# Kernel tuning notes

Measured on AMD Instinct MI355X. Metric: run time of the kernel, lower is better.

Reference implementation:

```python
import jax, jax.numpy as jnp
import numpy as np
import math

DIM_IN, DIM_CTX, DIM_KEY, DIM_VAL = 2048, 512, 128, 128
N, T, H, W = 8, 16, 32, 32
NBOX = 512


def setup_inputs() -> dict:
    key = jax.random.key(0)
    ks = jax.random.split(key, 10)
    rois = jax.random.normal(ks[0], (NBOX, DIM_IN), dtype=jnp.float32)
    context = jax.random.normal(ks[1], (N, DIM_CTX, T, H, W), dtype=jnp.float32)
    batch_idx = jnp.sort(jax.random.randint(ks[2], (NBOX,), 0, N))
    s = 0.02
    W_proj = jax.random.normal(ks[3], (DIM_KEY, DIM_IN), dtype=jnp.float32) * s
    b_proj = jnp.zeros((DIM_KEY,), dtype=jnp.float32)
    W_keys = jax.random.normal(ks[4], (DIM_KEY, DIM_CTX), dtype=jnp.float32) * s
    b_keys = jnp.zeros((DIM_KEY,), dtype=jnp.float32)
    W_vals = jax.random.normal(ks[5], (DIM_VAL, DIM_CTX), dtype=jnp.float32) * s
    b_vals = jnp.zeros((DIM_VAL,), dtype=jnp.float32)
    return {"rois": rois, "context": context, "batch_idx": batch_idx,
            "W_proj": W_proj, "b_proj": b_proj,
            "W_keys": W_keys, "b_keys": b_keys,
            "W_vals": W_vals, "b_vals": b_vals}


def reference(rois, context, batch_idx, W_proj, b_proj, W_keys, b_keys, W_vals, b_vals):
    n, c, t, h, w = context.shape
    s = t * h * w
    dk = W_keys.shape[0]
    # ROI query projection: [Nb, dk]
    q = rois @ W_proj.T + b_proj
    # 1x1x1 Conv3d == per-voxel linear over channels
    ctx_flat = context.reshape(n, c, s)                       # [N, C, S]
    keys = jnp.einsum('kc,ncs->nks', W_keys, ctx_flat) + b_keys[None, :, None]  # [N, dk, S]
    vals = jnp.einsum('vc,ncs->nsv', W_vals, ctx_flat) + b_vals[None, None, :]  # [N, S, dv]
    # Per-box gather of its clip's keys/vals, fused cross-attention
    qk = jnp.einsum('bk,bks->bs', q, keys[batch_idx]) / math.sqrt(dk)  # [Nb, S]
    coeff = jax.nn.softmax(qk, axis=-1)
    ctx_out = jnp.einsum('bs,bsv->bv', coeff, vals[batch_idx])         # [Nb, dv]
    attn = coeff.reshape(-1, t, h, w) * 255.0
    return ctx_out, attn
```

## Files before the change

### kernel.cpp

```cpp
#include <hip/hip_runtime.h>
#include <hip/hip_bf16.h>
#include <math.h>

#define DIM_IN  2048
#define DIM_CTX 512
#define DIM_KEY 128
#define DIM_VAL 128
#define NCLIP   8
#define S_TOT   16384
#define NBOX    512
#define MAXB    96

typedef __attribute__((ext_vector_type(8))) short short8_t;
typedef __attribute__((ext_vector_type(4))) float f32x4;

__device__ inline unsigned short f2bf(float x) {
    union { float f; unsigned int u; } v; v.f = x;
    unsigned int r = v.u + 0x7FFFu + ((v.u >> 16) & 1u);
    return (unsigned short)(r >> 16);
}
__device__ inline float bf2f(unsigned short h) {
    union { unsigned int u; float f; } v; v.u = ((unsigned int)h) << 16;
    return v.f;
}

__global__ __launch_bounds__(256) void k0_init(const int* __restrict__ batch_idx,
                                               int* __restrict__ ranges,
                                               float* __restrict__ cctx) {
    int idx = blockIdx.x * blockDim.x + threadIdx.x;
    for (int i = idx; i < NBOX * DIM_CTX; i += gridDim.x * blockDim.x)
        cctx[i] = 0.0f;
    if (blockIdx.x == 0) {
        __shared__ int s_start[NCLIP], s_end[NCLIP];
        if (threadIdx.x < NCLIP) { s_start[threadIdx.x] = NBOX; s_end[threadIdx.x] = 0; }
        __syncthreads();
        for (int i = threadIdx.x; i < NBOX; i += blockDim.x) {
            int b = batch_idx[i];
            atomicMin(&s_start[b], i);
            atomicMax(&s_end[b], i + 1);
        }
        __syncthreads();
        if (threadIdx.x < NCLIP) {
            ranges[threadIdx.x]         = s_start[threadIdx.x];
            ranges[NCLIP + threadIdx.x] = s_end[threadIdx.x];
        }
    }
}

__global__ __launch_bounds__(256) void conv_ctx(const float* __restrict__ ctx,
                                                unsigned short* __restrict__ ctxB,
                                                unsigned short* __restrict__ ctxT) {
    int n = blockIdx.z;
    int c0 = blockIdx.y * 64;
    int sch = blockIdx.x * 128;
    int t = threadIdx.x;
    __shared__ float ls[64 * 132];
    const float* src = ctx + ((size_t)n * DIM_CTX + c0) * S_TOT + sch;
    unsigned short* dstB = ctxB + ((size_t)n * DIM_CTX + c0) * S_TOT + sch;
    #pragma unroll
    for (int r = 0; r < 8; ++r) {
        int idx = t + r * 256;
        int c_l = idx >> 5, s4 = (idx & 31) * 4;
        float4 v = *(const float4*)(src + (size_t)c_l * S_TOT + s4);
        *(float4*)&ls[c_l * 132 + s4] = v;
        uint2 pk;
        pk.x = f2bf(v.x) | ((unsigned)f2bf(v.y) << 16);
        pk.y = f2bf(v.z) | ((unsigned)f2bf(v.w) << 16);
        *(uint2*)(dstB + (size_t)c_l * S_TOT + s4) = pk;
    }
    __syncthreads();
    int s_l = t >> 1, ch = (t & 1) * 32;
    unsigned int pk[16];
    #pragma unroll
    for (int i = 0; i < 16; ++i) {
        unsigned short h0 = f2bf(ls[(ch + 2 * i + 0) * 132 + s_l]);
        unsigned short h1 = f2bf(ls[(ch + 2 * i + 1) * 132 + s_l]);
        pk[i] = h0 | ((unsigned)h1 << 16);
    }
    unsigned short* dstT = ctxT + ((size_t)n * S_TOT + sch + s_l) * DIM_CTX + c0 + ch;
    #pragma unroll
    for (int i = 0; i < 4; ++i)
        ((uint4*)dstT)[i] = *(uint4*)&pk[i * 4];
}

__global__ __launch_bounds__(128) void k1a_q(const float* __restrict__ rois,
                                             const float* __restrict__ W_proj,
                                             const float* __restrict__ b_proj,
                                             float* __restrict__ q) {
    __shared__ float s_roi[4 * DIM_IN];
    int b0 = blockIdx.x * 4;
    const float4* src = (const float4*)(rois + (size_t)b0 * DIM_IN);
    for (int i = threadIdx.x; i < 4 * DIM_IN / 4; i += blockDim.x)
        ((float4*)s_roi)[i] = src[i];
    __syncthreads();
    int k = threadIdx.x;
    const float4* wrow = (const float4*)(W_proj + (size_t)k * DIM_IN);
    float a0 = 0.f, a1 = 0.f, a2 = 0.f, a3 = 0.f;
    for (int i = 0; i < DIM_IN / 4; ++i) {
        float4 w  = wrow[i];
        float4 r0 = *(const float4*)&s_roi[0 * DIM_IN + i * 4];
        float4 r1 = *(const float4*)&s_roi[1 * DIM_IN + i * 4];
        float4 r2 = *(const float4*)&s_roi[2 * DIM_IN + i * 4];
        float4 r3 = *(const float4*)&s_roi[3 * DIM_IN + i * 4];
        a0 += w.x * r0.x; a0 += w.y * r0.y; a0 += w.z * r0.z; a0 += w.w * r0.w;
        a1 += w.x * r1.x; a1 += w.y * r1.y; a1 += w.z * r1.z; a1 += w.w * r1.w;
        a2 += w.x * r2.x; a2 += w.y * r2.y; a2 += w.z * r2.z; a2 += w.w * r2.w;
        a3 += w.x * r3.x; a3 += w.y * r3.y; a3 += w.z * r3.z; a3 += w.w * r3.w;
    }
    float bp = b_proj[k];
    q[(size_t)(b0 + 0) * DIM_KEY + k] = a0 + bp;
    q[(size_t)(b0 + 1) * DIM_KEY + k] = a1 + bp;
    q[(size_t)(b0 + 2) * DIM_KEY + k] = a2 + bp;
    q[(size_t)(b0 + 3) * DIM_KEY + k] = a3 + bp;
}

__global__ __launch_bounds__(256) void k1b_qw(const float* __restrict__ q,
                                              const float* __restrict__ W_keys,
                                              const float* __restrict__ b_keys,
                                              unsigned short* __restrict__ qW_hi,
                                              unsigned short* __restrict__ qW_lo,
                                              float* __restrict__ qbias) {
    __shared__ float s_q[4 * DIM_KEY];
    __shared__ float red[256];
    int b0 = blockIdx.x * 4;
    for (int i = threadIdx.x; i < 4 * DIM_KEY; i += blockDim.x)
        s_q[i] = q[(size_t)b0 * DIM_KEY + i];
    __syncthreads();
    int c0 = threadIdx.x, c1 = threadIdx.x + 256;
    float a[4][2] = {{0.f,0.f},{0.f,0.f},{0.f,0.f},{0.f,0.f}};
    for (int k = 0; k < DIM_KEY; ++k) {
        float w0 = W_keys[(size_t)k * DIM_CTX + c0];
        float w1 = W_keys[(size_t)k * DIM_CTX + c1];
        float q0 = s_q[0 * DIM_KEY + k], q1 = s_q[1 * DIM_KEY + k];
        float q2 = s_q[2 * DIM_KEY + k], q3 = s_q[3 * DIM_KEY + k];
        a[0][0] += q0 * w0; a[0][1] += q0 * w1;
        a[1][0] += q1 * w0; a[1][1] += q1 * w1;
        a[2][0] += q2 * w0; a[2][1] += q2 * w1;
        a[3][0] += q3 * w0; a[3][1] += q3 * w1;
    }
    #pragma unroll
    for (int j = 0; j < 4; ++j) {
        #pragma unroll
        for (int cc = 0; cc < 2; ++cc) {
            int c = (cc == 0) ? c0 : c1;
            float x = a[j][cc];
            unsigned short h = f2bf(x);
            qW_hi[(size_t)(b0 + j) * DIM_CTX + c] = h;
            qW_lo[(size_t)(b0 + j) * DIM_CTX + c] = f2bf(x - bf2f(h));
        }
    }
    for (int j = 0; j < 4; ++j) {
        float v = 0.f;
        if (threadIdx.x < DIM_KEY) v = s_q[j * DIM_KEY + threadIdx.x] * b_keys[threadIdx.x];
        red[threadIdx.x] = v;
        __syncthreads();
        for (int st = 128; st > 0; st >>= 1) {
            if (threadIdx.x < st) red[threadIdx.x] += red[threadIdx.x + st];
            __syncthreads();
        }
        if (threadIdx.x == 0) qbias[b0 + j] = red[0];
        __syncthreads();
    }
}

__global__ __launch_bounds__(256) void k2_scores(
    const unsigned short* __restrict__ ctxT, const unsigned short* __restrict__ qW_hi,
    const unsigned short* __restrict__ qW_lo, const float* __restrict__ qbias,
    const int* __restrict__ ranges, float* __restrict__ scores)
{
    int n = blockIdx.y;
    int start = ranges[n], Mb = ranges[NCLIP + n] - start;
    if (Mb <= 0) return;
    const unsigned short* ctxTn = ctxT + (size_t)n * S_TOT * DIM_CTX;
    int sch = blockIdx.x * 128;
    int t = threadIdx.x, lane = t & 63, w = t >> 6;

    __shared__ unsigned short ls_b[128 * 64];
    __shared__ unsigned short ls_qh[MAXB * 64];
    __shared__ unsigned short ls_ql[MAXB * 64];

    for (int bp = 0; bp < Mb; bp += MAXB) {
        int nb = min(MAXB, Mb - bp);
        f32x4 acc[6][2];
        #pragma unroll
        for (int m = 0; m < 6; ++m)
            #pragma unroll
            for (int nn = 0; nn < 2; ++nn)
                acc[m][nn] = (f32x4){0.f, 0.f, 0.f, 0.f};

        for (int it = 0; it < 8; ++it) {
            int c0 = it * 64;
            __syncthreads();
            #pragma unroll
            for (int r = 0; r < 4; ++r) {
                int idx = t + r * 256;
                int s_l = idx >> 3, c8 = (idx & 7) * 8;
                uint4 v = *(const uint4*)(ctxTn + (size_t)(sch + s_l) * DIM_CTX + c0 + c8);
                *(uint4*)((char*)ls_b + ((s_l * 128 + c8 * 2) ^ ((s_l & 7) << 4))) = v;
            }
            for (int idx = t; idx < MAXB * 8; idx += 256) {
                int row = idx >> 3, c8 = (idx & 7) * 8;
                uint4 vh = {0,0,0,0}, vl = {0,0,0,0};
                if (row < nb) {
                    size_t go = (size_t)(start + bp + row) * DIM_CTX + c0 + c8;
                    vh = *(const uint4*)(qW_hi + go);
                    vl = *(const uint4*)(qW_lo + go);
                }
                int off = (row * 128 + c8 * 2) ^ ((row & 7) << 4);
                *(uint4*)((char*)ls_qh + off) = vh;
                *(uint4*)((char*)ls_ql + off) = vl;
            }
            __syncthreads();
            #pragma unroll
            for (int ks = 0; ks < 2; ++ks) {
                int hi16 = ks * 64 + (lane >> 4) * 16;
                short8_t Ah[6], Al[6], Bv[2];
                #pragma unroll
                for (int m = 0; m < 6; ++m) {
                    if (m * 16 < nb) {
                        int row = m * 16 + (lane & 15);
                        int off = (row * 128 + hi16) ^ ((row & 7) << 4);
                        Ah[m] = *(const short8_t*)((const char*)ls_qh + off);
                        Al[m] = *(const short8_t*)((const char*)ls_ql + off);
                    }
                }
                #pragma unroll
                for (int nn = 0; nn < 2; ++nn) {
                    int srow = (w * 2 + nn) * 16 + (lane & 15);
                    int off = (srow * 128 + hi16) ^ ((srow & 7) << 4);
                    Bv[nn] = *(const short8_t*)((const char*)ls_b + off);
                }
                #pragma unroll
                for (int m = 0; m < 6; ++m) {
                    if (m * 16 < nb) {
                        #pragma unroll
                        for (int nn = 0; nn < 2; ++nn) {
                            acc[m][nn] = __builtin_amdgcn_mfma_f32_16x16x32_bf16(Ah[m], Bv[nn], acc[m][nn], 0, 0, 0);
                            acc[m][nn] = __builtin_amdgcn_mfma_f32_16x16x32_bf16(Al[m], Bv[nn], acc[m][nn], 0, 0, 0);
                        }
                    }
                }
            }
        }
        const float rs = 0.08838834764831845f;
        #pragma unroll
        for (int m = 0; m < 6; ++m)
            #pragma unroll
            for (int r = 0; r < 4; ++r) {
                int b_l = m * 16 + ((lane >> 4) << 2) + r;
                if (b_l < nb) {
                    int bg = start + bp + b_l;
                    float qb = qbias[bg];
                    #pragma unroll
                    for (int nn = 0; nn < 2; ++nn) {
                        int s = sch + (w * 2 + nn) * 16 + (lane & 15);
                        scores[(size_t)bg * S_TOT + s] = (acc[m][nn][r] + qb) * rs;
                    }
                }
            }
        __syncthreads();
    }
}

__global__ __launch_bounds__(256) void k3_stats(const float* __restrict__ scores,
                                                float* __restrict__ rmax,
                                                float* __restrict__ rsum) {
    int b = blockIdx.x;
    const float4* row = (const float4*)(scores + (size_t)b * S_TOT);
    __shared__ float red[256];
    float mx = -1e30f;
    for (int i = threadIdx.x; i < S_TOT / 4; i += 256) {
        float4 v = row[i];
        mx = fmaxf(mx, fmaxf(fmaxf(v.x, v.y), fmaxf(v.z, v.w)));
    }
    red[threadIdx.x] = mx;
    __syncthreads();
    for (int st = 128; st > 0; st >>= 1) {
        if (threadIdx.x < st) red[threadIdx.x] = fmaxf(red[threadIdx.x], red[threadIdx.x + st]);
        __syncthreads();
    }
    mx = red[0];
    __syncthreads();
    float sm = 0.f;
    for (int i = threadIdx.x; i < S_TOT / 4; i += 256) {
        float4 v = row[i];
        sm += __expf(v.x - mx) + __expf(v.y - mx) + __expf(v.z - mx) + __expf(v.w - mx);
    }
    red[threadIdx.x] = sm;
    __syncthreads();
    for (int st = 128; st > 0; st >>= 1) {
        if (threadIdx.x < st) red[threadIdx.x] += red[threadIdx.x + st];
        __syncthreads();
    }
    if (threadIdx.x == 0) { rmax[b] = mx; rsum[b] = 1.0f / red[0]; }
}

__global__ __launch_bounds__(256) void k4_pv(
    const unsigned short* __restrict__ ctxB, const int* __restrict__ ranges,
    const float* __restrict__ rmax, const float* __restrict__ rsum,
    float* __restrict__ attn, float* __restrict__ cctx)
{
    int n = blockIdx.y;
    int start = ranges[n], Mb = ranges[NCLIP + n] - start;
    if (Mb <= 0) return;
    const unsigned short* ctxn = ctxB + (size_t)n * DIM_CTX * S_TOT;
    int sch = blockIdx.x * 256;
    int t = threadIdx.x, lane = t & 63, w = t >> 6;
    int mh = w >> 1, ns = w & 1;

    __shared__ unsigned short ls_p[MAXB * 256];
    __shared__ unsigned short ls_c[32 * 256];

    for (int bp = 0; bp < Mb; bp += MAXB) {
        int nb = min(MAXB, Mb - bp);
        bool a0v = (mh + 0) * 16 < nb;
        bool a1v = (mh + 2) * 16 < nb;
        bool a2v = (mh + 4) * 16 < nb;
        __syncthreads();
        for (int idx = t; idx < MAXB * 64; idx += 256) {
            int b_l = idx >> 6, s4 = (idx & 63) * 4;
            uint2 pk; pk.x = 0u; pk.y = 0u;
            if (b_l < nb) {
                int bg = start + bp + b_l;
                size_t off = (size_t)bg * S_TOT + sch + s4;
                float4 v = *(const float4*)(attn + off);
                float m = rmax[bg], r = rsum[bg];
                float4 p;
                p.x = __expf(v.x - m) * r; p.y = __expf(v.y - m) * r;
                p.z = __expf(v.z - m) * r; p.w = __expf(v.w - m) * r;
                float4 o;
                o.x = 255.f * p.x; o.y = 255.f * p.y; o.z = 255.f * p.z; o.w = 255.f * p.w;
                *(float4*)(attn + off) = o;
                pk.x = f2bf(p.x) | ((unsigned)f2bf(p.y) << 16);
                pk.y = f2bf(p.z) | ((unsigned)f2bf(p.w) << 16);
            }
            int off8 = (b_l * 512 + s4 * 2) ^ ((b_l & 7) << 4);
            *(uint2*)((char*)ls_p + off8) = pk;
        }
        __syncthreads();
        short8_t A[3][8];
        int hi16 = (lane >> 4) * 16;
        #pragma unroll
        for (int mi = 0; mi < 3; ++mi) {
            int tm = mh + 2 * mi;
            if (tm * 16 < nb) {
                int row = tm * 16 + (lane & 15);
                int sw = (row & 7) << 4;
                #pragma unroll
                for (int k = 0; k < 8; ++k) {
                    int off = (row * 512 + k * 64 + hi16) ^ sw;
                    A[mi][k] = *(const short8_t*)((const char*)ls_p + off);
                }
            }
        }
        for (int ct = 0; ct < 16; ++ct) {
            __syncthreads();
            #pragma unroll
            for (int r = 0; r < 4; ++r) {
                int idx = t + r * 256;
                int c_l = idx >> 5, s8 = (idx & 31) * 8;
                uint4 v = *(const uint4*)(ctxn + (size_t)(ct * 32 + c_l) * S_TOT + sch + s8);
                int off8 = (c_l * 512 + s8 * 2) ^ ((c_l & 7) << 4);
                *(uint4*)((char*)ls_c + off8) = v;
            }
            __syncthreads();
            f32x4 acc0 = (f32x4){0,0,0,0}, acc1 = (f32x4){0,0,0,0}, acc2 = (f32x4){0,0,0,0};
            int crow = ns * 16 + (lane & 15);
            int swc = (crow & 7) << 4;
            #pragma unroll
            for (int k = 0; k < 8; ++k) {
                int off = (crow * 512 + k * 64 + hi16) ^ swc;
                short8_t B = *(const short8_t*)((const char*)ls_c + off);
                if (a0v) acc0 = __builtin_amdgcn_mfma_f32_16x16x32_bf16(A[0][k], B, acc0, 0, 0, 0);
                if (a1v) acc1 = __builtin_amdgcn_mfma_f32_16x16x32_bf16(A[1][k], B, acc1, 0, 0, 0);
                if (a2v) acc2 = __builtin_amdgcn_mfma_f32_16x16x32_bf16(A[2][k], B, acc2, 0, 0, 0);
            }
            int cg = ct * 32 + ns * 16 + (lane & 15);
            #pragma unroll
            for (int r = 0; r < 4; ++r) {
                int br = ((lane >> 4) << 2) + r;
                int b0l = (mh + 0) * 16 + br;
                int b1l = (mh + 2) * 16 + br;
                int b2l = (mh + 4) * 16 + br;
                if (a0v && b0l < nb) atomicAdd(&cctx[(size_t)(start + bp + b0l) * DIM_CTX + cg], acc0[r]);
                if (a1v && b1l < nb) atomicAdd(&cctx[(size_t)(start + bp + b1l) * DIM_CTX + cg], acc1[r]);
                if (a2v && b2l < nb) atomicAdd(&cctx[(size_t)(start + bp + b2l) * DIM_CTX + cg], acc2[r]);
            }
        }
    }
}

__global__ __launch_bounds__(128) void k5_out(const float* __restrict__ cctx,
                                              const float* __restrict__ W_vals,
                                              const float* __restrict__ b_vals,
                                              float* __restrict__ out) {
    __shared__ float s_c[4 * DIM_CTX];
    int b0 = blockIdx.x * 4;
    const float4* src = (const float4*)(cctx + (size_t)b0 * DIM_CTX);
    for (int i = threadIdx.x; i < 4 * DIM_CTX / 4; i += blockDim.x)
        ((float4*)s_c)[i] = src[i];
    __syncthreads();
    int v = threadIdx.x;
    const float4* wrow = (const float4*)(W_vals + (size_t)v * DIM_CTX);
    float a0 = 0.f, a1 = 0.f, a2 = 0.f, a3 = 0.f;
    for (int i = 0; i < DIM_CTX / 4; ++i) {
        float4 w  = wrow[i];
        float4 c0v = *(const float4*)&s_c[0 * DIM_CTX + i * 4];
        float4 c1v = *(const float4*)&s_c[1 * DIM_CTX + i * 4];
        float4 c2v = *(const float4*)&s_c[2 * DIM_CTX + i * 4];
        float4 c3v = *(const float4*)&s_c[3 * DIM_CTX + i * 4];
        a0 += w.x * c0v.x; a0 += w.y * c0v.y; a0 += w.z * c0v.z; a0 += w.w * c0v.w;
        a1 += w.x * c1v.x; a1 += w.y * c1v.y; a1 += w.z * c1v.z; a1 += w.w * c1v.w;
        a2 += w.x * c2v.x; a2 += w.y * c2v.y; a2 += w.z * c2v.z; a2 += w.w * c2v.w;
        a3 += w.x * c3v.x; a3 += w.y * c3v.y; a3 += w.z * c3v.z; a3 += w.w * c3v.w;
    }
    float bb = b_vals[v];
    out[(size_t)(b0 + 0) * DIM_VAL + v] = a0 + bb;
    out[(size_t)(b0 + 1) * DIM_VAL + v] = a1 + bb;
    out[(size_t)(b0 + 2) * DIM_VAL + v] = a2 + bb;
    out[(size_t)(b0 + 3) * DIM_VAL + v] = a3 + bb;
}

extern "C" void kernel_launch(void* const* d_in, const int* in_sizes, int n_in,
                              void* d_out, int out_size, void* d_ws, size_t ws_size,
                              hipStream_t stream) {
    const float* rois      = (const float*)d_in[0];
    const float* context   = (const float*)d_in[1];
    const int*   batch_idx = (const int*)  d_in[2];
    const float* W_proj    = (const float*)d_in[3];
    const float* b_proj    = (const float*)d_in[4];
    const float* W_keys    = (const float*)d_in[5];
    const float* b_keys    = (const float*)d_in[6];
    const float* W_vals    = (const float*)d_in[7];
    const float* b_vals    = (const float*)d_in[8];

    float* out  = (float*)d_out;
    float* attn = out + NBOX * DIM_VAL;

    char* wsb = (char*)d_ws;
    int*   ranges = (int*)wsb;
    float* q      = (float*)(wsb + 128);
    float* qbias  = q + NBOX * DIM_KEY;
    float* rmaxp  = qbias + NBOX;
    float* rsump  = rmaxp + NBOX;
    float* cctx   = rsump + NBOX;
    unsigned short* qW_hi = (unsigned short*)(cctx + NBOX * DIM_CTX);
    unsigned short* qW_lo = qW_hi + NBOX * DIM_CTX;
    unsigned short* ctxB  = qW_lo + NBOX * DIM_CTX;
    unsigned short* ctxT  = ctxB + (size_t)NCLIP * DIM_CTX * S_TOT;

    k0_init  <<<dim3(64),        dim3(256), 0, stream>>>(batch_idx, ranges, cctx);
    conv_ctx <<<dim3(128, 8, 8), dim3(256), 0, stream>>>(context, ctxB, ctxT);
    k1a_q    <<<dim3(NBOX / 4),  dim3(128), 0, stream>>>(rois, W_proj, b_proj, q);
    k1b_qw   <<<dim3(NBOX / 4),  dim3(256), 0, stream>>>(q, W_keys, b_keys, qW_hi, qW_lo, qbias);
    k2_scores<<<dim3(128, 8),    dim3(256), 0, stream>>>(ctxT, qW_hi, qW_lo, qbias, ranges, attn);
    k3_stats <<<dim3(NBOX),      dim3(256), 0, stream>>>(attn, rmaxp, rsump);
    k4_pv    <<<dim3(64, 8),     dim3(256), 0, stream>>>(ctxB, ranges, rmaxp, rsump, attn, cctx);
    k5_out   <<<dim3(NBOX / 4),  dim3(128), 0, stream>>>(cctx, W_vals, b_vals, out);
}
```

Baseline: 695.9 us.

## Fuse context conversion into score kernel and compute softmax partials in-place

Removes the separate conv_ctx kernel: k2_scores now reads fp32 context directly, converts it to bf16 in shared memory for its transposed tile, and writes the bf16 ctxB copy on the first box pass. It also computes per-block row max/sum-exp partials so the k3 stats kernel no longer rereads the full score matrix; a small k3r reduces the 128 partials per box. Separately, k1a_q is split into more blocks of two boxes, and k4_pv widens its channel tile to 64 to halve atomic/tile loop iterations. The change trades extra shared memory in k2 (lower occupancy) for avoiding a full ctxT write/read and a full score reread.

```diff
diff --git a/kernel.cpp b/kernel.cpp
--- a/kernel.cpp
+++ b/kernel.cpp
@@ -47,71 +47,29 @@
     }
 }
 
-__global__ __launch_bounds__(256) void conv_ctx(const float* __restrict__ ctx,
-                                                unsigned short* __restrict__ ctxB,
-                                                unsigned short* __restrict__ ctxT) {
-    int n = blockIdx.z;
-    int c0 = blockIdx.y * 64;
-    int sch = blockIdx.x * 128;
-    int t = threadIdx.x;
-    __shared__ float ls[64 * 132];
-    const float* src = ctx + ((size_t)n * DIM_CTX + c0) * S_TOT + sch;
-    unsigned short* dstB = ctxB + ((size_t)n * DIM_CTX + c0) * S_TOT + sch;
-    #pragma unroll
-    for (int r = 0; r < 8; ++r) {
-        int idx = t + r * 256;
-        int c_l = idx >> 5, s4 = (idx & 31) * 4;
-        float4 v = *(const float4*)(src + (size_t)c_l * S_TOT + s4);
-        *(float4*)&ls[c_l * 132 + s4] = v;
-        uint2 pk;
-        pk.x = f2bf(v.x) | ((unsigned)f2bf(v.y) << 16);
-        pk.y = f2bf(v.z) | ((unsigned)f2bf(v.w) << 16);
-        *(uint2*)(dstB + (size_t)c_l * S_TOT + s4) = pk;
-    }
-    __syncthreads();
-    int s_l = t >> 1, ch = (t & 1) * 32;
-    unsigned int pk[16];
-    #pragma unroll
-    for (int i = 0; i < 16; ++i) {
-        unsigned short h0 = f2bf(ls[(ch + 2 * i + 0) * 132 + s_l]);
-        unsigned short h1 = f2bf(ls[(ch + 2 * i + 1) * 132 + s_l]);
-        pk[i] = h0 | ((unsigned)h1 << 16);
-    }
-    unsigned short* dstT = ctxT + ((size_t)n * S_TOT + sch + s_l) * DIM_CTX + c0 + ch;
-    #pragma unroll
-    for (int i = 0; i < 4; ++i)
-        ((uint4*)dstT)[i] = *(uint4*)&pk[i * 4];
-}
-
 __global__ __launch_bounds__(128) void k1a_q(const float* __restrict__ rois,
                                              const float* __restrict__ W_proj,
                                              const float* __restrict__ b_proj,
                                              float* __restrict__ q) {
-    __shared__ float s_roi[4 * DIM_IN];
-    int b0 = blockIdx.x * 4;
+    __shared__ float s_roi[2 * DIM_IN];
+    int b0 = blockIdx.x * 2;
     const float4* src = (const float4*)(rois + (size_t)b0 * DIM_IN);
-    for (int i = threadIdx.x; i < 4 * DIM_IN / 4; i += blockDim.x)
+    for (int i = threadIdx.x; i < 2 * DIM_IN / 4; i += blockDim.x)
         ((float4*)s_roi)[i] = src[i];
     __syncthreads();
     int k = threadIdx.x;
     const float4* wrow = (const float4*)(W_proj + (size_t)k * DIM_IN);
-    float a0 = 0.f, a1 = 0.f, a2 = 0.f, a3 = 0.f;
+    float a0 = 0.f, a1 = 0.f;
     for (int i = 0; i < DIM_IN / 4; ++i) {
         float4 w  = wrow[i];
         float4 r0 = *(const float4*)&s_roi[0 * DIM_IN + i * 4];
         float4 r1 = *(const float4*)&s_roi[1 * DIM_IN + i * 4];
-        float4 r2 = *(const float4*)&s_roi[2 * DIM_IN + i * 4];
-        float4 r3 = *(const float4*)&s_roi[3 * DIM_IN + i * 4];
         a0 += w.x * r0.x; a0 += w.y * r0.y; a0 += w.z * r0.z; a0 += w.w * r0.w;
         a1 += w.x * r1.x; a1 += w.y * r1.y; a1 += w.z * r1.z; a1 += w.w * r1.w;
-        a2 += w.x * r2.x; a2 += w.y * r2.y; a2 += w.z * r2.z; a2 += w.w * r2.w;
-        a3 += w.x * r3.x; a3 += w.y * r3.y; a3 += w.z * r3.z; a3 += w.w * r3.w;
     }
     float bp = b_proj[k];
     q[(size_t)(b0 + 0) * DIM_KEY + k] = a0 + bp;
     q[(size_t)(b0 + 1) * DIM_KEY + k] = a1 + bp;
-    q[(size_t)(b0 + 2) * DIM_KEY + k] = a2 + bp;
-    q[(size_t)(b0 + 3) * DIM_KEY + k] = a3 + bp;
 }
 
 __global__ __launch_bounds__(256) void k1b_qw(const float* __restrict__ q,
@@ -164,20 +122,25 @@
 }
 
 __global__ __launch_bounds__(256) void k2_scores(
-    const unsigned short* __restrict__ ctxT, const unsigned short* __restrict__ qW_hi,
-    const unsigned short* __restrict__ qW_lo, const float* __restrict__ qbias,
-    const int* __restrict__ ranges, float* __restrict__ scores)
+    const float* __restrict__ ctx, unsigned short* __restrict__ ctxB,
+    const unsigned short* __restrict__ qW_hi, const unsigned short* __restrict__ qW_lo,
+    const float* __restrict__ qbias, const int* __restrict__ ranges,
+    float* __restrict__ scores, float* __restrict__ pmax, float* __restrict__ psum)
 {
     int n = blockIdx.y;
     int start = ranges[n], Mb = ranges[NCLIP + n] - start;
     if (Mb <= 0) return;
-    const unsigned short* ctxTn = ctxT + (size_t)n * S_TOT * DIM_CTX;
+    const float* ctxn = ctx + (size_t)n * DIM_CTX * S_TOT;
+    unsigned short* ctxBn = ctxB + (size_t)n * DIM_CTX * S_TOT;
     int sch = blockIdx.x * 128;
     int t = threadIdx.x, lane = t & 63, w = t >> 6;
 
+    __shared__ float          ls_f[64 * 132];
     __shared__ unsigned short ls_b[128 * 64];
     __shared__ unsigned short ls_qh[MAXB * 64];
     __shared__ unsigned short ls_ql[MAXB * 64];
+    __shared__ float          red_mx[4][MAXB];
+    __shared__ float          red_sm[4][MAXB];
 
     for (int bp = 0; bp < Mb; bp += MAXB) {
         int nb = min(MAXB, Mb - bp);
@@ -192,11 +155,17 @@
             int c0 = it * 64;
             __syncthreads();
             #pragma unroll
-            for (int r = 0; r < 4; ++r) {
-                int idx = t + r * 256;
-                int s_l = idx >> 3, c8 = (idx & 7) * 8;
-                uint4 v = *(const uint4*)(ctxTn + (size_t)(sch + s_l) * DIM_CTX + c0 + c8);
-                *(uint4*)((char*)ls_b + ((s_l * 128 + c8 * 2) ^ ((s_l & 7) << 4))) = v;
+            for (int rep = 0; rep < 8; ++rep) {
+                int idx = t + rep * 256;
+                int c_l = idx >> 5, s4 = (idx & 31) * 4;
+                float4 v = *(const float4*)(ctxn + (size_t)(c0 + c_l) * S_TOT + sch + s4);
+                *(float4*)&ls_f[c_l * 132 + s4] = v;
+                if (bp == 0) {
+                    uint2 pk;
+                    pk.x = f2bf(v.x) | ((unsigned)f2bf(v.y) << 16);
+                    pk.y = f2bf(v.z) | ((unsigned)f2bf(v.w) << 16);
+                    *(uint2*)(ctxBn + (size_t)(c0 + c_l) * S_TOT + sch + s4) = pk;
+                }
             }
             for (int idx = t; idx < MAXB * 8; idx += 256) {
                 int row = idx >> 3, c8 = (idx & 7) * 8;
@@ -209,6 +178,22 @@
                 int off = (row * 128 + c8 * 2) ^ ((row & 7) << 4);
                 *(uint4*)((char*)ls_qh + off) = vh;
                 *(uint4*)((char*)ls_ql + off) = vl;
+            }
+            __syncthreads();
+            {
+                int s_l = t >> 1, ch = (t & 1) * 32;
+                unsigned int pk[16];
+                #pragma unroll
+                for (int i = 0; i < 16; ++i) {
+                    unsigned short h0 = f2bf(ls_f[(ch + 2 * i + 0) * 132 + s_l]);
+                    unsigned short h1 = f2bf(ls_f[(ch + 2 * i + 1) * 132 + s_l]);
+                    pk[i] = h0 | ((unsigned)h1 << 16);
+                }
+                int sw = (s_l & 7) << 4;
+                int base = s_l * 128 + ch * 2;
+                #pragma unroll
+                for (int i = 0; i < 4; ++i)
+                    *(uint4*)((char*)ls_b + ((base + i * 16) ^ sw)) = *(uint4*)&pk[i * 4];
             }
             __syncthreads();
             #pragma unroll
@@ -244,55 +229,67 @@
         }
         const float rs = 0.08838834764831845f;
         #pragma unroll
-        for (int m = 0; m < 6; ++m)
+        for (int m = 0; m < 6; ++m) {
+            if (m * 16 >= nb) continue;
             #pragma unroll
             for (int r = 0; r < 4; ++r) {
                 int b_l = m * 16 + ((lane >> 4) << 2) + r;
-                if (b_l < nb) {
-                    int bg = start + bp + b_l;
+                bool valid = b_l < nb;
+                int bg = start + bp + b_l;
+                float sc0, sc1;
+                if (valid) {
                     float qb = qbias[bg];
-                    #pragma unroll
-                    for (int nn = 0; nn < 2; ++nn) {
-                        int s = sch + (w * 2 + nn) * 16 + (lane & 15);
-                        scores[(size_t)bg * S_TOT + s] = (acc[m][nn][r] + qb) * rs;
-                    }
-                }
-            }
-        __syncthreads();
-    }
-}
-
-__global__ __launch_bounds__(256) void k3_stats(const float* __restrict__ scores,
-                                                float* __restrict__ rmax,
-                                                float* __restrict__ rsum) {
-    int b = blockIdx.x;
-    const float4* row = (const float4*)(scores + (size_t)b * S_TOT);
-    __shared__ float red[256];
-    float mx = -1e30f;
-    for (int i = threadIdx.x; i < S_TOT / 4; i += 256) {
-        float4 v = row[i];
-        mx = fmaxf(mx, fmaxf(fmaxf(v.x, v.y), fmaxf(v.z, v.w)));
-    }
-    red[threadIdx.x] = mx;
+                    sc0 = (acc[m][0][r] + qb) * rs;
+                    sc1 = (acc[m][1][r] + qb) * rs;
+                    int s0 = sch + (w * 2 + 0) * 16 + (lane & 15);
+                    scores[(size_t)bg * S_TOT + s0]      = sc0;
+                    scores[(size_t)bg * S_TOT + s0 + 16] = sc1;
+                } else {
+                    sc0 = sc1 = -1e30f;
+                }
+                float mx = fmaxf(sc0, sc1);
+                #pragma unroll
+                for (int d = 1; d < 16; d <<= 1) mx = fmaxf(mx, __shfl_xor(mx, d, 16));
+                float e = __expf(sc0 - mx) + __expf(sc1 - mx);
+                #pragma unroll
+                for (int d = 1; d < 16; d <<= 1) e += __shfl_xor(e, d, 16);
+                if ((lane & 15) == 0) { red_mx[w][b_l] = mx; red_sm[w][b_l] = e; }
+            }
+        }
+        __syncthreads();
+        if (t < MAXB && t < nb) {
+            float m0 = red_mx[0][t], m1 = red_mx[1][t], m2 = red_mx[2][t], m3 = red_mx[3][t];
+            float M = fmaxf(fmaxf(m0, m1), fmaxf(m2, m3));
+            float S = red_sm[0][t] * __expf(m0 - M) + red_sm[1][t] * __expf(m1 - M)
+                    + red_sm[2][t] * __expf(m2 - M) + red_sm[3][t] * __expf(m3 - M);
+            int bg = start + bp + t;
+            pmax[(size_t)bg * 128 + blockIdx.x] = M;
+            psum[(size_t)bg * 128 + blockIdx.x] = S;
+        }
+        __syncthreads();
+    }
+}
+
+__global__ __launch_bounds__(128) void k3r(const float* __restrict__ pmax,
+                                           const float* __restrict__ psum,
+                                           float* __restrict__ rmax,
+                                           float* __restrict__ rsum) {
+    int b = blockIdx.x, t = threadIdx.x;
+    float m = pmax[(size_t)b * 128 + t];
+    float s = psum[(size_t)b * 128 + t];
+    __shared__ float sm[2], ss[2];
+    float M = m;
+    #pragma unroll
+    for (int d = 1; d < 64; d <<= 1) M = fmaxf(M, __shfl_xor(M, d, 64));
+    if ((t & 63) == 0) sm[t >> 6] = M;
     __syncthreads();
-    for (int st = 128; st > 0; st >>= 1) {
-        if (threadIdx.x < st) red[threadIdx.x] = fmaxf(red[threadIdx.x], red[threadIdx.x + st]);
-        __syncthreads();
-    }
-    mx = red[0];
+    float Mg = fmaxf(sm[0], sm[1]);
+    float e = s * __expf(m - Mg);
+    #pragma unroll
+    for (int d = 1; d < 64; d <<= 1) e += __shfl_xor(e, d, 64);
+    if ((t & 63) == 0) ss[t >> 6] = e;
     __syncthreads();
-    float sm = 0.f;
-    for (int i = threadIdx.x; i < S_TOT / 4; i += 256) {
-        float4 v = row[i];
-        sm += __expf(v.x - mx) + __expf(v.y - mx) + __expf(v.z - mx) + __expf(v.w - mx);
-    }
-    red[threadIdx.x] = sm;
-    __syncthreads();
-    for (int st = 128; st > 0; st >>= 1) {
-        if (threadIdx.x < st) red[threadIdx.x] += red[threadIdx.x + st];
-        __syncthreads();
-    }
-    if (threadIdx.x == 0) { rmax[b] = mx; rsum[b] = 1.0f / red[0]; }
+    if (t == 0) { rmax[b] = Mg; rsum[b] = 1.0f / (ss[0] + ss[1]); }
 }
 
 __global__ __launch_bounds__(256) void k4_pv(
@@ -309,7 +306,7 @@
     int mh = w >> 1, ns = w & 1;
 
     __shared__ unsigned short ls_p[MAXB * 256];
-    __shared__ unsigned short ls_c[32 * 256];
+    __shared__ unsigned short ls_c[64 * 256];
 
     for (int bp = 0; bp < Mb; bp += MAXB) {
         int nb = min(MAXB, Mb - bp);
@@ -353,38 +350,49 @@
                 }
             }
         }
-        for (int ct = 0; ct < 16; ++ct) {
-            __syncthreads();
-            #pragma unroll
-            for (int r = 0; r < 4; ++r) {
+        for (int ct = 0; ct < 8; ++ct) {
+            __syncthreads();
+            #pragma unroll
+            for (int r = 0; r < 8; ++r) {
                 int idx = t + r * 256;
                 int c_l = idx >> 5, s8 = (idx & 31) * 8;
-                uint4 v = *(const uint4*)(ctxn + (size_t)(ct * 32 + c_l) * S_TOT + sch + s8);
+                uint4 v = *(const uint4*)(ctxn + (size_t)(ct * 64 + c_l) * S_TOT + sch + s8);
                 int off8 = (c_l * 512 + s8 * 2) ^ ((c_l & 7) << 4);
                 *(uint4*)((char*)ls_c + off8) = v;
             }
             __syncthreads();
-            f32x4 acc0 = (f32x4){0,0,0,0}, acc1 = (f32x4){0,0,0,0}, acc2 = (f32x4){0,0,0,0};
-            int crow = ns * 16 + (lane & 15);
-            int swc = (crow & 7) << 4;
-            #pragma unroll
-            for (int k = 0; k < 8; ++k) {
-                int off = (crow * 512 + k * 64 + hi16) ^ swc;
-                short8_t B = *(const short8_t*)((const char*)ls_c + off);
-                if (a0v) acc0 = __builtin_amdgcn_mfma_f32_16x16x32_bf16(A[0][k], B, acc0, 0, 0, 0);
-                if (a1v) acc1 = __builtin_amdgcn_mfma_f32_16x16x32_bf16(A[1][k], B, acc1, 0, 0, 0);
-                if (a2v) acc2 = __builtin_amdgcn_mfma_f32_16x16x32_bf16(A[2][k], B, acc2, 0, 0, 0);
-            }
-            int cg = ct * 32 + ns * 16 + (lane & 15);
-            #pragma unroll
-            for (int r = 0; r < 4; ++r) {
-                int br = ((lane >> 4) << 2) + r;
-                int b0l = (mh + 0) * 16 + br;
-                int b1l = (mh + 2) * 16 + br;
-                int b2l = (mh + 4) * 16 + br;
-                if (a0v && b0l < nb) atomicAdd(&cctx[(size_t)(start + bp + b0l) * DIM_CTX + cg], acc0[r]);
-                if (a1v && b1l < nb) atomicAdd(&cctx[(size_t)(start + bp + b1l) * DIM_CTX + cg], acc1[r]);
-                if (a2v && b2l < nb) atomicAdd(&cctx[(size_t)(start + bp + b2l) * DIM_CTX + cg], acc2[r]);
+            f32x4 acc[3][2];
+            #pragma unroll
+            for (int mi = 0; mi < 3; ++mi)
+                #pragma unroll
+                for (int cn = 0; cn < 2; ++cn)
+                    acc[mi][cn] = (f32x4){0,0,0,0};
+            #pragma unroll
+            for (int cn = 0; cn < 2; ++cn) {
+                int crow = (ns * 2 + cn) * 16 + (lane & 15);
+                int swc = (crow & 7) << 4;
+                #pragma unroll
+                for (int k = 0; k < 8; ++k) {
+                    int off = (crow * 512 + k * 64 + hi16) ^ swc;
+                    short8_t B = *(const short8_t*)((const char*)ls_c + off);
+                    if (a0v) acc[0][cn] = __builtin_amdgcn_mfma_f32_16x16x32_bf16(A[0][k], B, acc[0][cn], 0, 0, 0);
+                    if (a1v) acc[1][cn] = __builtin_amdgcn_mfma_f32_16x16x32_bf16(A[1][k], B, acc[1][cn], 0, 0, 0);
+                    if (a2v) acc[2][cn] = __builtin_amdgcn_mfma_f32_16x16x32_bf16(A[2][k], B, acc[2][cn], 0, 0, 0);
+                }
+            }
+            #pragma unroll
+            for (int cn = 0; cn < 2; ++cn) {
+                int cg = ct * 64 + (ns * 2 + cn) * 16 + (lane & 15);
+                #pragma unroll
+                for (int r = 0; r < 4; ++r) {
+                    int br = ((lane >> 4) << 2) + r;
+                    int b0l = (mh + 0) * 16 + br;
+                    int b1l = (mh + 2) * 16 + br;
+                    int b2l = (mh + 4) * 16 + br;
+                    if (a0v && b0l < nb) atomicAdd(&cctx[(size_t)(start + bp + b0l) * DIM_CTX + cg], acc[0][cn][r]);
+                    if (a1v && b1l < nb) atomicAdd(&cctx[(size_t)(start + bp + b1l) * DIM_CTX + cg], acc[1][cn][r]);
+                    if (a2v && b2l < nb) atomicAdd(&cctx[(size_t)(start + bp + b2l) * DIM_CTX + cg], acc[2][cn][r]);
+                }
             }
         }
     }
@@ -444,17 +452,17 @@
     float* rmaxp  = qbias + NBOX;
     float* rsump  = rmaxp + NBOX;
     float* cctx   = rsump + NBOX;
-    unsigned short* qW_hi = (unsigned short*)(cctx + NBOX * DIM_CTX);
+    float* pmaxp  = cctx + NBOX * DIM_CTX;
+    float* psump  = pmaxp + NBOX * 128;
+    unsigned short* qW_hi = (unsigned short*)(psump + NBOX * 128);
     unsigned short* qW_lo = qW_hi + NBOX * DIM_CTX;
     unsigned short* ctxB  = qW_lo + NBOX * DIM_CTX;
-    unsigned short* ctxT  = ctxB + (size_t)NCLIP * DIM_CTX * S_TOT;
-
-    k0_init  <<<dim3(64),        dim3(256), 0, stream>>>(batch_idx, ranges, cctx);
-    conv_ctx <<<dim3(128, 8, 8), dim3(256), 0, stream>>>(context, ctxB, ctxT);
-    k1a_q    <<<dim3(NBOX / 4),  dim3(128), 0, stream>>>(rois, W_proj, b_proj, q);
-    k1b_qw   <<<dim3(NBOX / 4),  dim3(256), 0, stream>>>(q, W_keys, b_keys, qW_hi, qW_lo, qbias);
-    k2_scores<<<dim3(128, 8),    dim3(256), 0, stream>>>(ctxT, qW_hi, qW_lo, qbias, ranges, attn);
-    k3_stats <<<dim3(NBOX),      dim3(256), 0, stream>>>(attn, rmaxp, rsump);
-    k4_pv    <<<dim3(64, 8),     dim3(256), 0, stream>>>(ctxB, ranges, rmaxp, rsump, attn, cctx);
-    k5_out   <<<dim3(NBOX / 4),  dim3(128), 0, stream>>>(cctx, W_vals, b_vals, out);
-}
+
+    k0_init  <<<dim3(64),       dim3(256), 0, stream>>>(batch_idx, ranges, cctx);
+    k1a_q    <<<dim3(NBOX / 2), dim3(128), 0, stream>>>(rois, W_proj, b_proj, q);
+    k1b_qw   <<<dim3(NBOX / 4), dim3(256), 0, stream>>>(q, W_keys, b_keys, qW_hi, qW_lo, qbias);
+    k2_scores<<<dim3(128, 8),   dim3(256), 0, stream>>>(context, ctxB, qW_hi, qW_lo, qbias, ranges, attn, pmaxp, psump);
+    k3r      <<<dim3(NBOX),     dim3(128), 0, stream>>>(pmaxp, psump, rmaxp, rsump);
+    k4_pv    <<<dim3(64, 8),    dim3(256), 0, stream>>>(ctxB, ranges, rmaxp, rsump, attn, cctx);
+    k5_out   <<<dim3(NBOX / 4), dim3(128), 0, stream>>>(cctx, W_vals, b_vals, out);
+}
```

Result: slower. 712.1 us (+2.3%).
